# Optimization experiments

Hardware: AMD Instinct MI355X
Metric: run time of the kernel (lower is better)

## Reference

```python
import jax, jax.numpy as jnp
import numpy as np

B, T, V, D = 64, 288, 24, 256
TOD_DIM, DOW_DIM, DOM_DIM, DOY_DIM = 128, 32, 32, 64  # sums to D


def setup_inputs() -> dict:
    key = jax.random.key(0)
    ks = jax.random.split(key, 10)
    features = jax.random.normal(ks[0], (B, T, V), dtype=jnp.float32)
    bar_in_day = jax.random.randint(ks[1], (B, T), 0, 288, dtype=jnp.int32)
    day_of_week = jax.random.randint(ks[2], (B,), 0, 5, dtype=jnp.int32)
    day_of_month = jax.random.randint(ks[3], (B,), 1, 32, dtype=jnp.int32)
    day_of_year = jax.random.randint(ks[4], (B,), 1, 367, dtype=jnp.int32)
    # Per-variable Linear(1, D): weight column w_v (D,), bias b_v (D,)
    W = jax.random.normal(ks[5], (V, D), dtype=jnp.float32) * (1.0)
    b = jax.random.normal(ks[6], (V, D), dtype=jnp.float32) * 0.02
    # Positional embedding tables
    tod_table = jax.random.normal(ks[7], (288, TOD_DIM), dtype=jnp.float32) * 0.02
    dow_table = jax.random.normal(ks[8], (7, DOW_DIM), dtype=jnp.float32) * 0.02
    k9, k10 = jax.random.split(ks[9])
    dom_table = jax.random.normal(k9, (32, DOM_DIM), dtype=jnp.float32) * 0.02
    doy_table = jax.random.normal(k10, (367, DOY_DIM), dtype=jnp.float32) * 0.02
    return dict(features=features, bar_in_day=bar_in_day, day_of_week=day_of_week,
                day_of_month=day_of_month, day_of_year=day_of_year,
                W=W, b=b, tod_table=tod_table, dow_table=dow_table,
                dom_table=dom_table, doy_table=doy_table)


def reference(features, bar_in_day, day_of_week, day_of_month, day_of_year,
              W, b, tod_table, dow_table, dom_table, doy_table):
    # Variable embedding: 24 Linear(1->D) fused into one broadcast MAC
    # out[b,t,v,d] = x[b,t,v] * W[v,d] + b[v,d]
    emb = features[..., None] * W[None, None] + b[None, None]  # (B,T,V,D)
    # Composite positional encoding -> (B,T,D)
    tod = tod_table[bar_in_day]                                 # (B,T,TOD_DIM)
    Bsz, Tlen = bar_in_day.shape
    dow = jnp.broadcast_to(dow_table[day_of_week][:, None, :], (Bsz, Tlen, DOW_DIM))
    dom = jnp.broadcast_to(dom_table[day_of_month][:, None, :], (Bsz, Tlen, DOM_DIM))
    doy = jnp.broadcast_to(doy_table[day_of_year][:, None, :], (Bsz, Tlen, DOY_DIM))
    pos = jnp.concatenate([tod, dow, dom, doy], axis=-1)        # (B,T,D)
    # Broadcast add across V (pos unsqueezed at variable dim); dropout in eval mode (identity)
    return emb + pos[:, :, None, :]
```

## Files before the change

### kernel.cpp

```cpp
#include <hip/hip_runtime.h>

#define B_  64
#define T_  288
#define V_  24
#define D_  256
#define TOD_DIM 128
#define DOW_DIM 32
#define DOM_DIM 32
#define DOY_DIM 64

__global__ __launch_bounds__(256) void input_emb_kernel(
    const float* __restrict__ features,
    const int*   __restrict__ bar_in_day,
    const int*   __restrict__ day_of_week,
    const int*   __restrict__ day_of_month,
    const int*   __restrict__ day_of_year,
    const float* __restrict__ W,
    const float* __restrict__ bias,
    const float* __restrict__ tod_table,
    const float* __restrict__ dow_table,
    const float* __restrict__ dom_table,
    const float* __restrict__ doy_table,
    float* __restrict__ out)
{
    __shared__ __align__(16) float pos[D_];
    __shared__ float feats[V_];

    const int bt  = blockIdx.x;
    const int b   = bt / T_;
    const int tid = threadIdx.x;

    {
        const int d = tid;
        float p;
        if (d < TOD_DIM) {
            p = tod_table[bar_in_day[bt] * TOD_DIM + d];
        } else if (d < TOD_DIM + DOW_DIM) {
            p = dow_table[day_of_week[b] * DOW_DIM + (d - TOD_DIM)];
        } else if (d < TOD_DIM + DOW_DIM + DOM_DIM) {
            p = dom_table[day_of_month[b] * DOM_DIM + (d - TOD_DIM - DOW_DIM)];
        } else {
            p = doy_table[day_of_year[b] * DOY_DIM + (d - TOD_DIM - DOW_DIM - DOM_DIM)];
        }
        pos[d] = p;
    }
    if (tid < V_) feats[tid] = features[bt * V_ + tid];
    __syncthreads();

    float* outbt = out + (size_t)bt * (V_ * D_);

    #pragma unroll
    for (int it = 0; it < (V_ * D_ / 4) / 256; ++it) {
        const int idx = it * 256 + tid;
        const int v   = idx >> 6;
        const int d4  = idx & 63;

        const float x = feats[v];
        const float4 w4 = *reinterpret_cast<const float4*>(W    + (v << 8) + (d4 << 2));
        const float4 b4 = *reinterpret_cast<const float4*>(bias + (v << 8) + (d4 << 2));
        const float4 p4 = *reinterpret_cast<const float4*>(&pos[d4 << 2]);

        float4 o;
        o.x = fmaf(x, w4.x, b4.x) + p4.x;
        o.y = fmaf(x, w4.y, b4.y) + p4.y;
        o.z = fmaf(x, w4.z, b4.z) + p4.z;
        o.w = fmaf(x, w4.w, b4.w) + p4.w;

        *reinterpret_cast<float4*>(outbt + (idx << 2)) = o;
    }
}

extern "C" void kernel_launch(void* const* d_in, const int* in_sizes, int n_in,
                              void* d_out, int out_size, void* d_ws, size_t ws_size,
                              hipStream_t stream) {
    const float* features     = (const float*)d_in[0];
    const int*   bar_in_day   = (const int*)d_in[1];
    const int*   day_of_week  = (const int*)d_in[2];
    const int*   day_of_month = (const int*)d_in[3];
    const int*   day_of_year  = (const int*)d_in[4];
    const float* W            = (const float*)d_in[5];
    const float* bias         = (const float*)d_in[6];
    const float* tod_table    = (const float*)d_in[7];
    const float* dow_table    = (const float*)d_in[8];
    const float* dom_table    = (const float*)d_in[9];
    const float* doy_table    = (const float*)d_in[10];
    float* out = (float*)d_out;

    dim3 grid(B_ * T_);
    dim3 block(256);
    input_emb_kernel<<<grid, block, 0, stream>>>(
        features, bar_in_day, day_of_week, day_of_month, day_of_year,
        W, bias, tod_table, dow_table, dom_table, doy_table, out);
}
```

Before: 85.32 us.

## Process four timesteps per block and use nontemporal output stores

Each block now handles four (b,t) positions instead of one. W and bias float4 values are loaded once and reused across the four positions, and each thread keeps its positional vectors in registers. Output writes switch to nontemporal stores so the large streaming output bypasses cache retention. The per-block position setup assumes the four timesteps share the same batch index, which holds because T is divisible by 4. The grid has a quarter as many blocks and each thread holds more registers.

```diff
diff --git a/kernel.cpp b/kernel.cpp
--- a/kernel.cpp
+++ b/kernel.cpp
@@ -8,6 +8,9 @@
 #define DOW_DIM 32
 #define DOM_DIM 32
 #define DOY_DIM 64
+#define BTPB 4
+
+typedef float f32x4 __attribute__((ext_vector_type(4)));
 
 __global__ __launch_bounds__(256) void input_emb_kernel(
     const float* __restrict__ features,
@@ -23,50 +26,63 @@
     const float* __restrict__ doy_table,
     float* __restrict__ out)
 {
-    __shared__ __align__(16) float pos[D_];
-    __shared__ float feats[V_];
+    __shared__ __align__(16) float pos[BTPB][D_];
+    __shared__ float feats[BTPB][V_];
 
-    const int bt  = blockIdx.x;
-    const int b   = bt / T_;
+    const int bt0 = blockIdx.x * BTPB;
+    const int b   = bt0 / T_;
     const int tid = threadIdx.x;
 
-    {
-        const int d = tid;
+    if (tid < TOD_DIM) {
+        #pragma unroll
+        for (int j = 0; j < BTPB; ++j)
+            pos[j][tid] = tod_table[bar_in_day[bt0 + j] * TOD_DIM + tid];
+    } else {
         float p;
-        if (d < TOD_DIM) {
-            p = tod_table[bar_in_day[bt] * TOD_DIM + d];
-        } else if (d < TOD_DIM + DOW_DIM) {
-            p = dow_table[day_of_week[b] * DOW_DIM + (d - TOD_DIM)];
-        } else if (d < TOD_DIM + DOW_DIM + DOM_DIM) {
-            p = dom_table[day_of_month[b] * DOM_DIM + (d - TOD_DIM - DOW_DIM)];
+        if (tid < TOD_DIM + DOW_DIM) {
+            p = dow_table[day_of_week[b] * DOW_DIM + (tid - TOD_DIM)];
+        } else if (tid < TOD_DIM + DOW_DIM + DOM_DIM) {
+            p = dom_table[day_of_month[b] * DOM_DIM + (tid - TOD_DIM - DOW_DIM)];
         } else {
-            p = doy_table[day_of_year[b] * DOY_DIM + (d - TOD_DIM - DOW_DIM - DOM_DIM)];
+            p = doy_table[day_of_year[b] * DOY_DIM + (tid - TOD_DIM - DOW_DIM - DOM_DIM)];
         }
-        pos[d] = p;
+        #pragma unroll
+        for (int j = 0; j < BTPB; ++j)
+            pos[j][tid] = p;
     }
-    if (tid < V_) feats[tid] = features[bt * V_ + tid];
+    if (tid < BTPB * V_) {
+        feats[tid / V_][tid % V_] = features[bt0 * V_ + tid];
+    }
     __syncthreads();
 
-    float* outbt = out + (size_t)bt * (V_ * D_);
+    const int d4 = tid & 63;
+    const int q  = tid >> 6;
+
+    f32x4 p4[BTPB];
+    #pragma unroll
+    for (int j = 0; j < BTPB; ++j)
+        p4[j] = *reinterpret_cast<const f32x4*>(&pos[j][d4 << 2]);
+
+    float* outbase = out + (size_t)bt0 * (V_ * D_);
 
     #pragma unroll
-    for (int it = 0; it < (V_ * D_ / 4) / 256; ++it) {
-        const int idx = it * 256 + tid;
-        const int v   = idx >> 6;
-        const int d4  = idx & 63;
+    for (int it = 0; it < V_ / 4; ++it) {
+        const int v = it * 4 + q;
+        const f32x4 w4 = *reinterpret_cast<const f32x4*>(W    + (v << 8) + (d4 << 2));
+        const f32x4 b4 = *reinterpret_cast<const f32x4*>(bias + (v << 8) + (d4 << 2));
+        const int idx = (v << 6) + d4;
 
-        const float x = feats[v];
-        const float4 w4 = *reinterpret_cast<const float4*>(W    + (v << 8) + (d4 << 2));
-        const float4 b4 = *reinterpret_cast<const float4*>(bias + (v << 8) + (d4 << 2));
-        const float4 p4 = *reinterpret_cast<const float4*>(&pos[d4 << 2]);
-
-        float4 o;
-        o.x = fmaf(x, w4.x, b4.x) + p4.x;
-        o.y = fmaf(x, w4.y, b4.y) + p4.y;
-        o.z = fmaf(x, w4.z, b4.z) + p4.z;
-        o.w = fmaf(x, w4.w, b4.w) + p4.w;
-
-        *reinterpret_cast<float4*>(outbt + (idx << 2)) = o;
+        #pragma unroll
+        for (int j = 0; j < BTPB; ++j) {
+            const float x = feats[j][v];
+            f32x4 o;
+            o.x = fmaf(x, w4.x, b4.x) + p4[j].x;
+            o.y = fmaf(x, w4.y, b4.y) + p4[j].y;
+            o.z = fmaf(x, w4.z, b4.z) + p4[j].z;
+            o.w = fmaf(x, w4.w, b4.w) + p4[j].w;
+            __builtin_nontemporal_store(o,
+                reinterpret_cast<f32x4*>(outbase + (size_t)j * (V_ * D_) + (idx << 2)));
+        }
     }
 }
 
@@ -86,7 +102,7 @@
     const float* doy_table    = (const float*)d_in[10];
     float* out = (float*)d_out;
 
-    dim3 grid(B_ * T_);
+    dim3 grid((B_ * T_) / BTPB);
     dim3 block(256);
     input_emb_kernel<<<grid, block, 0, stream>>>(
         features, bar_in_day, day_of_week, day_of_month, day_of_year,
```

Result: slower. 92.22 us (+8.1%).
